# Optimization experiments

Hardware: AMD Instinct MI355X
Metric: run time of the kernel (lower is better)

The kernel has to match this reference:

```python
import jax, jax.numpy as jnp
import numpy as np


def setup_inputs() -> dict:
    key = jax.random.key(0)
    k1, k2, k3 = jax.random.split(key, 3)
    B, C, D = 4096, 10000, 512
    feat = jax.random.normal(k1, (B, D), dtype=jnp.float32)
    label = jax.random.randint(k2, (B,), 0, C, dtype=jnp.int64)
    # xavier_uniform for weights [C, D]: bound = sqrt(6/(C+D))
    bound = np.sqrt(6.0 / (C + D)).astype(np.float32)
    weights = jax.random.uniform(k3, (C, D), dtype=jnp.float32, minval=-bound, maxval=bound)
    return {"feat": feat, "label": label, "weights": weights}


def reference(feat, label, weights):
    # pairwise squared L2 distance between feat [B,D] and weights [C,D]
    # computed via the Gram-matrix identity (same math as broadcast-sub-square-sum)
    f2 = jnp.sum(feat * feat, axis=-1, keepdims=True)          # [B,1]
    w2 = jnp.sum(weights * weights, axis=-1)[None, :]          # [1,C]
    cross = jnp.einsum('bd,cd->bc', feat, weights)             # [B,C]
    metric = jnp.maximum(f2 + w2 - 2.0 * cross, 0.0)           # [B,C] sq dists
    kernal_metric = jnp.exp(-0.01 * metric)                    # RBF kernel logits
    # original computes avg kernel value at true labels but then overrides
    # scale = 1.0, so logits are just the kernel values
    scale = 1.0
    train_logits = scale * kernal_metric
    valuation_logits = scale * kernal_metric
    return (train_logits, valuation_logits, weights)
```

## Files before the change

kernel.cpp:

```cpp
#include <hip/hip_runtime.h>
#include <hip/hip_bf16.h>
#include <stdint.h>

#define BDIM 4096
#define CDIM 10000
#define DDIM 512
#define CPAD 10112
#define NT 16

typedef __bf16 bf16_t;
typedef __attribute__((ext_vector_type(2))) __bf16 bf16x2;
typedef __attribute__((ext_vector_type(8))) __bf16 bf16x8;
typedef __attribute__((ext_vector_type(2))) float f32x2;
typedef __attribute__((ext_vector_type(4))) float f32x4;

__device__ __forceinline__ void gl_lds16(const void* g, void* s) {
  __builtin_amdgcn_global_load_lds(
      (const __attribute__((address_space(1))) void*)g,
      (__attribute__((address_space(3))) void*)s, 16, 0, 0);
}

__global__ __launch_bounds__(256) void prep(
    const float* __restrict__ feat, const float* __restrict__ w,
    bf16_t* __restrict__ fb, bf16_t* __restrict__ wb,
    float* __restrict__ f2, float* __restrict__ w2,
    float* __restrict__ wout) {
  const int b = blockIdx.x;
  const int t = threadIdx.x;
  __shared__ float red[4];
  if (b < BDIM) {
    const f32x2 v = ((const f32x2*)(feat + (size_t)b * DDIM))[t];
    bf16x2 o;
    o.x = (__bf16)v.x;
    o.y = (__bf16)v.y;
    ((bf16x2*)fb)[(size_t)b * (DDIM / 2) + t] = o;
    float ss = v.x * v.x + v.y * v.y;
#pragma unroll
    for (int off = 32; off > 0; off >>= 1) ss += __shfl_down(ss, off);
    if ((t & 63) == 0) red[t >> 6] = ss;
    __syncthreads();
    if (t == 0) f2[b] = red[0] + red[1] + red[2] + red[3];
  } else {
    const int row = b - BDIM;
    if (row < CDIM) {
      const f32x2 v = ((const f32x2*)(w + (size_t)row * DDIM))[t];
      __builtin_nontemporal_store(v, (f32x2*)(wout + (size_t)row * DDIM) + t);
      bf16x2 o;
      o.x = (__bf16)v.x;
      o.y = (__bf16)v.y;
      ((bf16x2*)wb)[(size_t)row * (DDIM / 2) + t] = o;
      float ss = v.x * v.x + v.y * v.y;
#pragma unroll
      for (int off = 32; off > 0; off >>= 1) ss += __shfl_down(ss, off);
      if ((t & 63) == 0) red[t >> 6] = ss;
      __syncthreads();
      if (t == 0) w2[row] = red[0] + red[1] + red[2] + red[3];
    } else {
      bf16x2 z;
      z.x = (__bf16)0.0f;
      z.y = (__bf16)0.0f;
      ((bf16x2*)wb)[(size_t)row * (DDIM / 2) + t] = z;
      if (t == 0) w2[row] = 0.0f;
    }
  }
}

__global__ __launch_bounds__(256, 3) void rbf_gemm(
    const bf16_t* __restrict__ A,
    const bf16_t* __restrict__ Bw,
    const float* __restrict__ f2g, const float* __restrict__ w2g,
    float* __restrict__ out) {
  __shared__ __align__(16) char pool[49152];
  bf16_t* At = (bf16_t*)pool;
  bf16_t* Bt = (bf16_t*)(pool + 24576);
  __shared__ float f2s[128];
  __shared__ float w2s[128];

  const int bid = blockIdx.x;
  const int wg = (bid & 7) * (2528 / 8) + (bid >> 3);
  const int bm = wg & 31;
  const int bn = wg >> 5;
  const int t = threadIdx.x;
  const int lane = t & 63;

  if (t < 128)
    f2s[t] = f2g[bm * 128 + t];
  else
    w2s[t - 128] = w2g[bn * 128 + (t - 128)];

  const int sr = t >> 2;
  const int sc = (t & 3) * 8;
  const bf16_t* ga0 = A + (size_t)(bm * 128 + sr) * DDIM + sc;
  const bf16_t* ga1 = ga0 + (size_t)64 * DDIM;
  const bf16_t* gb0 = Bw + (size_t)(bn * 128 + sr) * DDIM + sc;
  const bf16_t* gb1 = gb0 + (size_t)64 * DDIM;

  const int wv = t >> 6;
  const int wm = (wv >> 1) * 64;
  const int wn = (wv & 1) * 64;
  const int fr = lane & 15;
  const int k8 = (lane >> 4) * 8;

#define STAGE(boff, kt)                              \
  do {                                               \
    const int k0_ = (kt) * 32;                       \
    gl_lds16(ga0 + k0_, At + (boff) + t * 8);        \
    gl_lds16(ga1 + k0_, At + (boff) + 2048 + t * 8); \
    gl_lds16(gb0 + k0_, Bt + (boff) + t * 8);        \
    gl_lds16(gb1 + k0_, Bt + (boff) + 2048 + t * 8); \
  } while (0)

  f32x4 acc[4][4];
#pragma unroll
  for (int i = 0; i < 4; ++i)
#pragma unroll
    for (int j = 0; j < 4; ++j) acc[i][j] = (f32x4){0.f, 0.f, 0.f, 0.f};

  STAGE(0, 0);
  STAGE(4096, 1);
  __syncthreads();

  int o0 = 0, o1 = 4096, o2 = 8192;
#pragma unroll
  for (int kt = 0; kt < NT; ++kt) {
    if (kt + 2 < NT) STAGE(o2, kt + 2);
    bf16x8 af[4], wf[4];
#pragma unroll
    for (int mi = 0; mi < 4; ++mi)
      af[mi] = *(const bf16x8*)(At + o0 + (wm + mi * 16 + fr) * 32 + k8);
#pragma unroll
    for (int ni = 0; ni < 4; ++ni)
      wf[ni] = *(const bf16x8*)(Bt + o0 + (wn + ni * 16 + fr) * 32 + k8);
    __builtin_amdgcn_s_setprio(1);
#pragma unroll
    for (int mi = 0; mi < 4; ++mi)
#pragma unroll
      for (int ni = 0; ni < 4; ++ni)
        acc[mi][ni] = __builtin_amdgcn_mfma_f32_16x16x32_bf16(
            wf[ni], af[mi], acc[mi][ni], 0, 0, 0);
    __builtin_amdgcn_s_setprio(0);
    if (kt < NT - 1) {
      if (kt + 2 < NT)
        asm volatile("s_waitcnt vmcnt(4)" ::: "memory");
      else
        asm volatile("s_waitcnt vmcnt(0)" ::: "memory");
      __builtin_amdgcn_s_barrier();
    }
    const int tmp = o0;
    o0 = o1;
    o1 = o2;
    o2 = tmp;
  }

  __syncthreads();

  float* resh = (float*)pool;
  const size_t BC = (size_t)BDIM * CDIM;
  const int m_l = lane & 15;
  const int c_l = (lane >> 4) * 4;

  for (int p = 0; p < 2; ++p) {
    if ((wv >> 1) == p) {
#pragma unroll
      for (int mi = 0; mi < 4; ++mi) {
        const int rl = mi * 16 + m_l;
        const float frow = f2s[wm + rl];
#pragma unroll
        for (int ni = 0; ni < 4; ++ni) {
          const int cl = wn + ni * 16 + c_l;
          f32x4 st;
#pragma unroll
          for (int j = 0; j < 4; ++j) {
            float m = frow + w2s[cl + j] - 2.0f * acc[mi][ni][j];
            m = fmaxf(m, 0.0f);
            st[j] = __expf(-0.01f * m);
          }
          *(f32x4*)(resh + rl * 132 + cl) = st;
        }
      }
    }
    __syncthreads();
    {
      const int rr = t >> 5;
      const int cc = (t & 31) * 4;
      const int gcol = bn * 128 + cc;
      if (gcol < CDIM) {
#pragma unroll
        for (int it = 0; it < 8; ++it) {
          const int r = it * 8 + rr;
          const f32x4 v = *(const f32x4*)(resh + r * 132 + cc);
          float* orow = out + (size_t)(bm * 128 + p * 64 + r) * CDIM + gcol;
          __builtin_nontemporal_store(v, (f32x4*)orow);
          __builtin_nontemporal_store(v, (f32x4*)(orow + BC));
        }
      }
    }
    __syncthreads();
  }
#undef STAGE
}

extern "C" void kernel_launch(void* const* d_in, const int* in_sizes, int n_in,
                              void* d_out, int out_size, void* d_ws,
                              size_t ws_size, hipStream_t stream) {
  const float* feat = (const float*)d_in[0];
  const float* w = (const float*)d_in[2];
  float* out = (float*)d_out;

  char* ws = (char*)d_ws;
  bf16_t* fb = (bf16_t*)ws;
  bf16_t* wb = (bf16_t*)(ws + 4194304);
  float* f2 = (float*)(ws + 4194304 + 10354688);
  float* w2 = (float*)(ws + 4194304 + 10354688 + 16384);

  float* wout = out + (size_t)2 * BDIM * CDIM;

  prep<<<BDIM + CPAD, 256, 0, stream>>>(feat, w, fb, wb, f2, w2, wout);
  rbf_gemm<<<2528, 256, 0, stream>>>(fb, wb, f2, w2, out);
}
```

Baseline: 115.0 us.

## Switch GEMM to double-buffered LDS with XOR-swizzled epilogue to raise occupancy

Reduces the LDS pipeline from three stages (48KB) to two (32KB) so the launch bound can rise from three to four blocks per CU. Loads for the next k-tile now overlap only one compute step and are waited on with a full __syncthreads instead of a partial vmcnt wait. The epilogue staging buffer drops its row padding and uses an XOR swizzle on column groups to avoid bank conflicts while fitting in the smaller pool. The risk is less prefetch depth and a full barrier per iteration, which may expose memory latency.

After: 109.8 us. -4.5%, faster.

```diff
diff --git a/kernel.cpp b/kernel.cpp
--- a/kernel.cpp
+++ b/kernel.cpp
@@ -65,14 +65,13 @@
   }
 }
 
-__global__ __launch_bounds__(256, 3) void rbf_gemm(
+__global__ __launch_bounds__(256, 4) void rbf_gemm(
     const bf16_t* __restrict__ A,
     const bf16_t* __restrict__ Bw,
     const float* __restrict__ f2g, const float* __restrict__ w2g,
     float* __restrict__ out) {
-  __shared__ __align__(16) char pool[49152];
-  bf16_t* At = (bf16_t*)pool;
-  bf16_t* Bt = (bf16_t*)(pool + 24576);
+  __shared__ __align__(16) char pool[32768];
+  bf16_t* Pb = (bf16_t*)pool;
   __shared__ float f2s[128];
   __shared__ float w2s[128];
 
@@ -101,13 +100,14 @@
   const int fr = lane & 15;
   const int k8 = (lane >> 4) * 8;
 
-#define STAGE(boff, kt)                              \
-  do {                                               \
-    const int k0_ = (kt) * 32;                       \
-    gl_lds16(ga0 + k0_, At + (boff) + t * 8);        \
-    gl_lds16(ga1 + k0_, At + (boff) + 2048 + t * 8); \
-    gl_lds16(gb0 + k0_, Bt + (boff) + t * 8);        \
-    gl_lds16(gb1 + k0_, Bt + (boff) + 2048 + t * 8); \
+#define STAGE(b, kt)                                         \
+  do {                                                       \
+    const int k0_ = (kt) * 32;                               \
+    bf16_t* Ab_ = Pb + (b) * 8192;                           \
+    gl_lds16(ga0 + k0_, Ab_ + t * 8);                        \
+    gl_lds16(ga1 + k0_, Ab_ + 2048 + t * 8);                 \
+    gl_lds16(gb0 + k0_, Ab_ + 4096 + t * 8);                 \
+    gl_lds16(gb1 + k0_, Ab_ + 4096 + 2048 + t * 8);          \
   } while (0)
 
   f32x4 acc[4][4];
@@ -117,20 +117,20 @@
     for (int j = 0; j < 4; ++j) acc[i][j] = (f32x4){0.f, 0.f, 0.f, 0.f};
 
   STAGE(0, 0);
-  STAGE(4096, 1);
   __syncthreads();
 
-  int o0 = 0, o1 = 4096, o2 = 8192;
 #pragma unroll
   for (int kt = 0; kt < NT; ++kt) {
-    if (kt + 2 < NT) STAGE(o2, kt + 2);
+    const int cur = kt & 1;
+    if (kt + 1 < NT) STAGE(cur ^ 1, kt + 1);
+    const bf16_t* Ab = Pb + cur * 8192;
     bf16x8 af[4], wf[4];
 #pragma unroll
     for (int mi = 0; mi < 4; ++mi)
-      af[mi] = *(const bf16x8*)(At + o0 + (wm + mi * 16 + fr) * 32 + k8);
+      af[mi] = *(const bf16x8*)(Ab + (wm + mi * 16 + fr) * 32 + k8);
 #pragma unroll
     for (int ni = 0; ni < 4; ++ni)
-      wf[ni] = *(const bf16x8*)(Bt + o0 + (wn + ni * 16 + fr) * 32 + k8);
+      wf[ni] = *(const bf16x8*)(Ab + 4096 + (wn + ni * 16 + fr) * 32 + k8);
     __builtin_amdgcn_s_setprio(1);
 #pragma unroll
     for (int mi = 0; mi < 4; ++mi)
@@ -139,17 +139,7 @@
         acc[mi][ni] = __builtin_amdgcn_mfma_f32_16x16x32_bf16(
             wf[ni], af[mi], acc[mi][ni], 0, 0, 0);
     __builtin_amdgcn_s_setprio(0);
-    if (kt < NT - 1) {
-      if (kt + 2 < NT)
-        asm volatile("s_waitcnt vmcnt(4)" ::: "memory");
-      else
-        asm volatile("s_waitcnt vmcnt(0)" ::: "memory");
-      __builtin_amdgcn_s_barrier();
-    }
-    const int tmp = o0;
-    o0 = o1;
-    o1 = o2;
-    o2 = tmp;
+    if (kt + 1 < NT) __syncthreads();
   }
 
   __syncthreads();
@@ -175,7 +165,7 @@
             m = fmaxf(m, 0.0f);
             st[j] = __expf(-0.01f * m);
           }
-          *(f32x4*)(resh + rl * 132 + cl) = st;
+          *(f32x4*)(resh + rl * 128 + (((cl >> 2) ^ (rl & 31)) << 2)) = st;
         }
       }
     }
@@ -188,7 +178,8 @@
 #pragma unroll
         for (int it = 0; it < 8; ++it) {
           const int r = it * 8 + rr;
-          const f32x4 v = *(const f32x4*)(resh + r * 132 + cc);
+          const f32x4 v =
+              *(const f32x4*)(resh + r * 128 + (((cc >> 2) ^ (r & 31)) << 2));
           float* orow = out + (size_t)(bm * 128 + p * 64 + r) * CDIM + gcol;
           __builtin_nontemporal_store(v, (f32x4*)orow);
           __builtin_nontemporal_store(v, (f32x4*)(orow + BC));
```
